# Kernel tuning notes

Measured on AMD Instinct MI355X. Metric: run time of the kernel, lower is better.

The kernel has to match this reference:

```python
import jax, jax.numpy as jnp
import numpy as np

N_NODES = 100000
N_EDGES = 3200000
D = 32


def setup_inputs() -> dict:
    key = jax.random.key(0)
    k = jax.random.split(key, 5)
    x = jax.random.normal(k[0], (N_NODES, D), dtype=jnp.float32)
    edge_index = jax.random.randint(k[1], (2, N_EDGES), 0, N_NODES, dtype=jnp.int64)
    W1 = jax.random.normal(k[2], (D, D), dtype=jnp.float32) * (1.0 / np.sqrt(D))
    b1 = jnp.zeros((D,), dtype=jnp.float32)
    W2 = jax.random.normal(k[3], (D, D), dtype=jnp.float32) * (1.0 / np.sqrt(D))
    b2 = jnp.zeros((D,), dtype=jnp.float32)
    return {"x": x, "edge_index": edge_index, "W1": W1, "b1": b1, "W2": W2, "b2": b2}


def reference(x, edge_index, W1, b1, W2, b2):
    n = x.shape[0]
    # add self-loops (PyG GCNConv default)
    loop = jnp.arange(n, dtype=edge_index.dtype)
    src = jnp.concatenate([edge_index[0], loop])
    dst = jnp.concatenate([edge_index[1], loop])
    # symmetric normalization: deg computed on dst with self-loops; deg >= 1 so no inf handling needed
    deg = jax.ops.segment_sum(jnp.ones_like(src, dtype=x.dtype), dst, num_segments=n)
    dinv = jax.lax.rsqrt(deg)
    norm = (dinv[src] * dinv[dst])[:, None]  # [E+N, 1]

    def gcn_layer(h, W, b):
        h = h @ W.T                                        # dense transform [N, D]
        msg = h[src] * norm                                # gather + scale   [E+N, D]
        agg = jax.ops.segment_sum(msg, dst, num_segments=n)  # scatter-add  [N, D]
        return jax.nn.relu(agg + b)

    h = gcn_layer(x, W1, b1)
    h = gcn_layer(h, W2, b2)
    return h
```

## Files before the change

### kernel.cpp

```cpp
#include <hip/hip_runtime.h>

#define THREADS 256
#define BIGT 1024
#define NBLK 256
#define BSHIFT 8
#define BSZ (1 << BSHIFT)
#define MAXB 512

__global__ void detect_kernel(const unsigned int* ei_words, int* flag_int64, long long n_words) {
    __shared__ int nonzero;
    if (threadIdx.x == 0) nonzero = 0;
    __syncthreads();
    long long w = 2LL * threadIdx.x + 1;
    if (w < n_words) {
        if (ei_words[w] != 0u) atomicOr(&nonzero, 1);
    }
    __syncthreads();
    if (threadIdx.x == 0) *flag_int64 = (nonzero == 0) ? 1 : 0;
}

__global__ __launch_bounds__(BIGT) void bin_count_kernel(
        const void* __restrict__ ei, const int* __restrict__ flag_int64,
        int* __restrict__ blockhist, int E, int NB) {
    __shared__ int h[MAXB];
    int tid = threadIdx.x;
    for (int i = tid; i < NB; i += blockDim.x) h[i] = 0;
    __syncthreads();
    int chunk = (E + gridDim.x - 1) / gridDim.x;
    int s = blockIdx.x * chunk;
    int e = min(E, s + chunk);
    if (*flag_int64) {
        const long long* p = (const long long*)ei;
        for (int i = s + tid; i < e; i += blockDim.x)
            atomicAdd(&h[(int)p[E + i] >> BSHIFT], 1);
    } else {
        const int* p = (const int*)ei;
        for (int i = s + tid; i < e; i += blockDim.x)
            atomicAdd(&h[p[E + i] >> BSHIFT], 1);
    }
    __syncthreads();
    for (int i = tid; i < NB; i += blockDim.x)
        blockhist[i * NBLK + blockIdx.x] = h[i];
}

__global__ __launch_bounds__(BIGT) void bin_write_kernel(
        const void* __restrict__ ei, const int* __restrict__ flag_int64,
        const int* __restrict__ offsets, unsigned int* __restrict__ ebuf,
        int E, int NB) {
    __shared__ int cur[MAXB];
    int tid = threadIdx.x;
    for (int i = tid; i < NB; i += blockDim.x)
        cur[i] = offsets[i * NBLK + blockIdx.x];
    __syncthreads();
    int chunk = (E + gridDim.x - 1) / gridDim.x;
    int s = blockIdx.x * chunk;
    int e = min(E, s + chunk);
    if (*flag_int64) {
        const long long* p = (const long long*)ei;
        for (int i = s + tid; i < e; i += blockDim.x) {
            int d = (int)p[E + i];
            int sr = (int)p[i];
            int pos = atomicAdd(&cur[d >> BSHIFT], 1);
            ebuf[pos] = ((unsigned int)(d & (BSZ - 1)) << 20) | (unsigned int)sr;
        }
    } else {
        const int* p = (const int*)ei;
        for (int i = s + tid; i < e; i += blockDim.x) {
            int d = p[E + i];
            int sr = p[i];
            int pos = atomicAdd(&cur[d >> BSHIFT], 1);
            ebuf[pos] = ((unsigned int)(d & (BSZ - 1)) << 20) | (unsigned int)sr;
        }
    }
}

__global__ void scan_blocks_kernel(const int* __restrict__ cnt, int* __restrict__ ofs,
                                   int* __restrict__ partials, int T) {
    __shared__ int sd[THREADS];
    int tid = threadIdx.x;
    int base = blockIdx.x * 1024 + tid * 4;
    int c0 = (base + 0 < T) ? cnt[base + 0] : 0;
    int c1 = (base + 1 < T) ? cnt[base + 1] : 0;
    int c2 = (base + 2 < T) ? cnt[base + 2] : 0;
    int c3 = (base + 3 < T) ? cnt[base + 3] : 0;
    int tsum = c0 + c1 + c2 + c3;
    sd[tid] = tsum;
    __syncthreads();
    for (int off = 1; off < THREADS; off <<= 1) {
        int t = (tid >= off) ? sd[tid - off] : 0;
        __syncthreads();
        sd[tid] += t;
        __syncthreads();
    }
    int excl = sd[tid] - tsum;
    if (base + 0 < T) ofs[base + 0] = excl;
    if (base + 1 < T) ofs[base + 1] = excl + c0;
    if (base + 2 < T) ofs[base + 2] = excl + c0 + c1;
    if (base + 3 < T) ofs[base + 3] = excl + c0 + c1 + c2;
    if (tid == THREADS - 1) partials[blockIdx.x] = sd[tid];
}

__global__ void scan_add2_kernel(int* __restrict__ ofs, const int* __restrict__ partials,
                                 int T, int SB) {
    __shared__ int sd[128];
    int tid = threadIdx.x;
    if (tid < 128) sd[tid] = (tid < SB) ? partials[tid] : 0;
    __syncthreads();
    for (int off = 1; off < 128; off <<= 1) {
        int t = (tid < 128 && tid >= off) ? sd[tid - off] : 0;
        __syncthreads();
        if (tid < 128) sd[tid] += t;
        __syncthreads();
    }
    int add = (blockIdx.x > 0) ? sd[blockIdx.x - 1] : 0;
    int base = blockIdx.x * 1024 + tid * 4;
    if (base + 0 < T) ofs[base + 0] += add;
    if (base + 1 < T) ofs[base + 1] += add;
    if (base + 2 < T) ofs[base + 2] += add;
    if (base + 3 < T) ofs[base + 3] += add;
    if (blockIdx.x == gridDim.x - 1 && tid == 0) ofs[T] = sd[SB - 1];
}

__global__ __launch_bounds__(BIGT) void place_dense_kernel(
        const unsigned int* __restrict__ ebuf, const int* __restrict__ offsets,
        const float* __restrict__ x, const float* __restrict__ W1,
        int* __restrict__ rowptr, float* __restrict__ dinv, int* __restrict__ col,
        float* __restrict__ ht1, int N, int NB) {
    __shared__ int cnt[BSZ];
    __shared__ int scanbuf[BSZ];
    __shared__ int baseL[BSZ];
    __shared__ int fillL[BSZ];
    __shared__ float dinvL[BSZ];
    __shared__ float Wt[1024];
    __shared__ float xs[BIGT];
    int b = blockIdx.x;
    int lo = b << BSHIFT;
    int tid = threadIdx.x;
    if (tid < BSZ) cnt[tid] = 0;
    Wt[(tid & 31) * 32 + (tid >> 5)] = W1[tid];
    __syncthreads();
    int start = offsets[b * NBLK];
    int end   = offsets[(b + 1) * NBLK];
    for (int p = start + tid; p < end; p += BIGT)
        atomicAdd(&cnt[(ebuf[p] >> 20) & (BSZ - 1)], 1);
    __syncthreads();
    int c = (tid < BSZ) ? cnt[tid] : 0;
    if (tid < BSZ) scanbuf[tid] = c;
    __syncthreads();
    for (int off = 1; off < BSZ; off <<= 1) {
        int t = (tid < BSZ && tid >= off) ? scanbuf[tid - off] : 0;
        __syncthreads();
        if (tid < BSZ) scanbuf[tid] += t;
        __syncthreads();
    }
    if (tid < BSZ) {
        int excl = scanbuf[tid] - c;
        int node = lo + tid;
        float dv = 1.0f / sqrtf((float)(c + 1));
        dinvL[tid] = dv;
        if (node < N) {
            rowptr[node] = start + excl;
            dinv[node] = dv;
            if (node == N - 1) rowptr[N] = start + excl + c;
        }
        baseL[tid] = start + excl;
        fillL[tid] = 0;
    }
    __syncthreads();
    for (int p = start + tid; p < end; p += BIGT) {
        unsigned int v = ebuf[p];
        int dl = (v >> 20) & (BSZ - 1);
        int pos = baseL[dl] + atomicAdd(&fillL[dl], 1);
        col[pos] = (int)(v & 0xFFFFFu);
    }
    __syncthreads();
    for (int base0 = 0; base0 < BSZ * 32; base0 += BIGT) {
        int idx = base0 + tid;
        int ln = idx >> 5;
        int node = lo + ln;
        xs[tid] = (node < N) ? x[(size_t)lo * 32 + idx] : 0.f;
        __syncthreads();
        if (node < N) {
            int j = idx & 31;
            const float* xr = xs + ((tid >> 5) << 5);
            float s = 0.f;
#pragma unroll
            for (int k = 0; k < 32; ++k) s = fmaf(xr[k], Wt[k * 32 + j], s);
            ht1[(size_t)node * 32 + j] = s * dinvL[ln];
        }
        __syncthreads();
    }
}

__global__ __launch_bounds__(THREADS) void agg_dense_kernel(
        const float* __restrict__ ht1, const int* __restrict__ rowptr,
        const int* __restrict__ col, const float* __restrict__ dinv,
        const float* __restrict__ b1, const float* __restrict__ W2,
        float* __restrict__ ht2, int N) {
    __shared__ float Wt[1024];
    __shared__ float hr[THREADS];
    int tid = threadIdx.x;
    for (int idx = tid; idx < 1024; idx += THREADS)
        Wt[(idx & 31) * 32 + (idx >> 5)] = W2[idx];
    int gid = blockIdx.x * THREADS + tid;
    int n = gid >> 5;
    int j = gid & 31;
    bool act = (n < N);
    float h1v = 0.f, dv = 0.f;
    if (act) {
        dv = dinv[n];
        float s = ht1[gid];
        int p = rowptr[n], end = rowptr[n + 1];
        for (; p + 8 <= end; p += 8) {
            int c0 = col[p], c1 = col[p + 1], c2 = col[p + 2], c3 = col[p + 3];
            int c4 = col[p + 4], c5 = col[p + 5], c6 = col[p + 6], c7 = col[p + 7];
            float v0 = ht1[c0 * 32 + j];
            float v1 = ht1[c1 * 32 + j];
            float v2 = ht1[c2 * 32 + j];
            float v3 = ht1[c3 * 32 + j];
            float v4 = ht1[c4 * 32 + j];
            float v5 = ht1[c5 * 32 + j];
            float v6 = ht1[c6 * 32 + j];
            float v7 = ht1[c7 * 32 + j];
            s += ((v0 + v1) + (v2 + v3)) + ((v4 + v5) + (v6 + v7));
        }
        for (; p + 4 <= end; p += 4) {
            int c0 = col[p], c1 = col[p + 1], c2 = col[p + 2], c3 = col[p + 3];
            float v0 = ht1[c0 * 32 + j];
            float v1 = ht1[c1 * 32 + j];
            float v2 = ht1[c2 * 32 + j];
            float v3 = ht1[c3 * 32 + j];
            s += (v0 + v1) + (v2 + v3);
        }
        for (; p < end; ++p) s += ht1[col[p] * 32 + j];
        h1v = fmaxf(fmaf(dv, s, b1[j]), 0.f);
    }
    hr[tid] = h1v;
    __syncthreads();
    if (act) {
        const float* hrow = hr + ((tid >> 5) << 5);
        float t = 0.f;
#pragma unroll
        for (int k = 0; k < 32; ++k) t = fmaf(hrow[k], Wt[k * 32 + j], t);
        ht2[gid] = t * dv;
    }
}

__global__ __launch_bounds__(THREADS) void agg_final_kernel(
        const float* __restrict__ ht2, const int* __restrict__ rowptr,
        const int* __restrict__ col, const float* __restrict__ dinv,
        const float* __restrict__ bias, float* __restrict__ out, int N) {
    int gid = blockIdx.x * THREADS + threadIdx.x;
    int n = gid >> 5;
    if (n >= N) return;
    int j = gid & 31;
    float s = ht2[gid];
    int p = rowptr[n], end = rowptr[n + 1];
    for (; p + 8 <= end; p += 8) {
        int c0 = col[p], c1 = col[p + 1], c2 = col[p + 2], c3 = col[p + 3];
        int c4 = col[p + 4], c5 = col[p + 5], c6 = col[p + 6], c7 = col[p + 7];
        float v0 = ht2[c0 * 32 + j];
        float v1 = ht2[c1 * 32 + j];
        float v2 = ht2[c2 * 32 + j];
        float v3 = ht2[c3 * 32 + j];
        float v4 = ht2[c4 * 32 + j];
        float v5 = ht2[c5 * 32 + j];
        float v6 = ht2[c6 * 32 + j];
        float v7 = ht2[c7 * 32 + j];
        s += ((v0 + v1) + (v2 + v3)) + ((v4 + v5) + (v6 + v7));
    }
    for (; p + 4 <= end; p += 4) {
        int c0 = col[p], c1 = col[p + 1], c2 = col[p + 2], c3 = col[p + 3];
        float v0 = ht2[c0 * 32 + j];
        float v1 = ht2[c1 * 32 + j];
        float v2 = ht2[c2 * 32 + j];
        float v3 = ht2[c3 * 32 + j];
        s += (v0 + v1) + (v2 + v3);
    }
    for (; p < end; ++p) s += ht2[col[p] * 32 + j];
    float r = fmaxf(fmaf(dinv[n], s, bias[j]), 0.f);
    __builtin_nontemporal_store(r, out + gid);
}

extern "C" void kernel_launch(void* const* d_in, const int* in_sizes, int n_in,
                              void* d_out, int out_size, void* d_ws, size_t ws_size,
                              hipStream_t stream) {
    const float* x  = (const float*)d_in[0];
    const void*  ei = d_in[1];
    const float* W1 = (const float*)d_in[2];
    const float* b1 = (const float*)d_in[3];
    const float* W2 = (const float*)d_in[4];
    const float* b2 = (const float*)d_in[5];
    float* out = (float*)d_out;

    int N = in_sizes[0] / 32;
    long long twoE = (long long)in_sizes[1];
    int E = (int)(twoE / 2);
    int NB = (N + BSZ - 1) >> BSHIFT;
    int T  = NB * NBLK;

    char* ws = (char*)d_ws;
    size_t o = 0;
    auto alloc = [&](size_t bytes) { size_t r = o; o += (bytes + 255) & ~(size_t)255; return r; };
    int*   flag      = (int*)(ws + alloc(4));
    int*   blockhist = (int*)(ws + alloc((size_t)T * 4));
    int*   offsets   = (int*)(ws + alloc((size_t)(T + 1) * 4));
    int*   rowptr    = (int*)(ws + alloc((size_t)(N + 1) * 4));
    int*   partials  = (int*)(ws + alloc(512));
    float* dinv      = (float*)(ws + alloc((size_t)N * 4));
    unsigned int* ebuf = (unsigned int*)(ws + alloc((size_t)E * 4));
    int*   col       = (int*)(ws + alloc((size_t)E * 4));
    float* ht1       = (float*)(ws + alloc((size_t)N * 32 * 4));
    float* ht2       = (float*)(ws + alloc((size_t)N * 32 * 4));

    detect_kernel<<<1, 256, 0, stream>>>((const unsigned int*)ei, flag, twoE);

    bin_count_kernel<<<NBLK, BIGT, 0, stream>>>(ei, flag, blockhist, E, NB);

    int SB = (T + 1023) / 1024;
    scan_blocks_kernel<<<SB, THREADS, 0, stream>>>(blockhist, offsets, partials, T);
    scan_add2_kernel<<<SB, THREADS, 0, stream>>>(offsets, partials, T, SB);

    bin_write_kernel<<<NBLK, BIGT, 0, stream>>>(ei, flag, offsets, ebuf, E, NB);
    place_dense_kernel<<<NB, BIGT, 0, stream>>>(ebuf, offsets, x, W1, rowptr, dinv, col, ht1, N, NB);

    int GB = (N * 32 + THREADS - 1) / THREADS;
    agg_dense_kernel<<<GB, THREADS, 0, stream>>>(ht1, rowptr, col, dinv, b1, W2, ht2, N);
    agg_final_kernel<<<GB, THREADS, 0, stream>>>(ht2, rowptr, col, dinv, b2, out, N);
}
```

Before: 274.7 us.

## Fold dtype probe and partial-scan add into binning kernels, unroll gathers to 16

Removes the separate int64-detect kernel by probing the high words inside each binning block, and removes the scan-add kernel by having consumer kernels rescan the block partials in LDS and add them on the fly. This cuts two kernel launches and one pass over the offsets array. The aggregation loops are also unrolled to 16 gathers per iteration to raise memory-level parallelism, at the cost of more registers. The per-block dtype probe only checks that block's own chunk, which could disagree across blocks in edge cases.

```diff
diff --git a/kernel.cpp b/kernel.cpp
--- a/kernel.cpp
+++ b/kernel.cpp
@@ -6,30 +6,28 @@
 #define BSHIFT 8
 #define BSZ (1 << BSHIFT)
 #define MAXB 512
-
-__global__ void detect_kernel(const unsigned int* ei_words, int* flag_int64, long long n_words) {
-    __shared__ int nonzero;
-    if (threadIdx.x == 0) nonzero = 0;
-    __syncthreads();
-    long long w = 2LL * threadIdx.x + 1;
-    if (w < n_words) {
-        if (ei_words[w] != 0u) atomicOr(&nonzero, 1);
-    }
-    __syncthreads();
-    if (threadIdx.x == 0) *flag_int64 = (nonzero == 0) ? 1 : 0;
+#define MAXSB 128
+
+__device__ __forceinline__ bool probe_int64(const void* ei, int s, int e, int tid, int* nz) {
+    if (tid == 0) *nz = 0;
+    __syncthreads();
+    int i = s + tid;
+    if (i < e && ((const unsigned int*)ei)[2 * i + 1] != 0u) atomicOr(nz, 1);
+    __syncthreads();
+    return (*nz == 0);
 }
 
 __global__ __launch_bounds__(BIGT) void bin_count_kernel(
-        const void* __restrict__ ei, const int* __restrict__ flag_int64,
-        int* __restrict__ blockhist, int E, int NB) {
+        const void* __restrict__ ei, int* __restrict__ blockhist, int E, int NB) {
     __shared__ int h[MAXB];
+    __shared__ int nz;
     int tid = threadIdx.x;
     for (int i = tid; i < NB; i += blockDim.x) h[i] = 0;
-    __syncthreads();
     int chunk = (E + gridDim.x - 1) / gridDim.x;
     int s = blockIdx.x * chunk;
     int e = min(E, s + chunk);
-    if (*flag_int64) {
+    bool is64 = probe_int64(ei, s, e, tid, &nz);
+    if (is64) {
         const long long* p = (const long long*)ei;
         for (int i = s + tid; i < e; i += blockDim.x)
             atomicAdd(&h[(int)p[E + i] >> BSHIFT], 1);
@@ -43,19 +41,63 @@
         blockhist[i * NBLK + blockIdx.x] = h[i];
 }
 
+__global__ void scan_blocks_kernel(const int* __restrict__ cnt, int* __restrict__ ofs,
+                                   int* __restrict__ partials, int T) {
+    __shared__ int sd[THREADS];
+    int tid = threadIdx.x;
+    int base = blockIdx.x * 1024 + tid * 4;
+    int c0 = (base + 0 < T) ? cnt[base + 0] : 0;
+    int c1 = (base + 1 < T) ? cnt[base + 1] : 0;
+    int c2 = (base + 2 < T) ? cnt[base + 2] : 0;
+    int c3 = (base + 3 < T) ? cnt[base + 3] : 0;
+    int tsum = c0 + c1 + c2 + c3;
+    sd[tid] = tsum;
+    __syncthreads();
+    for (int off = 1; off < THREADS; off <<= 1) {
+        int t = (tid >= off) ? sd[tid - off] : 0;
+        __syncthreads();
+        sd[tid] += t;
+        __syncthreads();
+    }
+    int excl = sd[tid] - tsum;
+    if (base + 0 < T) ofs[base + 0] = excl;
+    if (base + 1 < T) ofs[base + 1] = excl + c0;
+    if (base + 2 < T) ofs[base + 2] = excl + c0 + c1;
+    if (base + 3 < T) ofs[base + 3] = excl + c0 + c1 + c2;
+    if (tid == THREADS - 1) partials[blockIdx.x] = sd[tid];
+}
+
+__device__ __forceinline__ void scan_partials_lds(const int* __restrict__ partials,
+                                                  int* pscan, int tid, int SB) {
+    if (tid < MAXSB) pscan[tid] = (tid < SB) ? partials[tid] : 0;
+    __syncthreads();
+    for (int off = 1; off < MAXSB; off <<= 1) {
+        int t = (tid < MAXSB && tid >= off) ? pscan[tid - off] : 0;
+        __syncthreads();
+        if (tid < MAXSB) pscan[tid] += t;
+        __syncthreads();
+    }
+}
+
 __global__ __launch_bounds__(BIGT) void bin_write_kernel(
-        const void* __restrict__ ei, const int* __restrict__ flag_int64,
-        const int* __restrict__ offsets, unsigned int* __restrict__ ebuf,
-        int E, int NB) {
+        const void* __restrict__ ei, const int* __restrict__ ofs_local,
+        const int* __restrict__ partials, unsigned int* __restrict__ ebuf,
+        int E, int NB, int SB) {
     __shared__ int cur[MAXB];
-    int tid = threadIdx.x;
-    for (int i = tid; i < NB; i += blockDim.x)
-        cur[i] = offsets[i * NBLK + blockIdx.x];
-    __syncthreads();
+    __shared__ int pscan[MAXSB];
+    __shared__ int nz;
+    int tid = threadIdx.x;
+    scan_partials_lds(partials, pscan, tid, SB);
+    for (int i = tid; i < NB; i += blockDim.x) {
+        int idx = i * NBLK + blockIdx.x;
+        int c = idx >> 10;
+        cur[i] = ((c > 0) ? pscan[c - 1] : 0) + ofs_local[idx];
+    }
     int chunk = (E + gridDim.x - 1) / gridDim.x;
     int s = blockIdx.x * chunk;
     int e = min(E, s + chunk);
-    if (*flag_int64) {
+    bool is64 = probe_int64(ei, s, e, tid, &nz);
+    if (is64) {
         const long long* p = (const long long*)ei;
         for (int i = s + tid; i < e; i += blockDim.x) {
             int d = (int)p[E + i];
@@ -74,58 +116,12 @@
     }
 }
 
-__global__ void scan_blocks_kernel(const int* __restrict__ cnt, int* __restrict__ ofs,
-                                   int* __restrict__ partials, int T) {
-    __shared__ int sd[THREADS];
-    int tid = threadIdx.x;
-    int base = blockIdx.x * 1024 + tid * 4;
-    int c0 = (base + 0 < T) ? cnt[base + 0] : 0;
-    int c1 = (base + 1 < T) ? cnt[base + 1] : 0;
-    int c2 = (base + 2 < T) ? cnt[base + 2] : 0;
-    int c3 = (base + 3 < T) ? cnt[base + 3] : 0;
-    int tsum = c0 + c1 + c2 + c3;
-    sd[tid] = tsum;
-    __syncthreads();
-    for (int off = 1; off < THREADS; off <<= 1) {
-        int t = (tid >= off) ? sd[tid - off] : 0;
-        __syncthreads();
-        sd[tid] += t;
-        __syncthreads();
-    }
-    int excl = sd[tid] - tsum;
-    if (base + 0 < T) ofs[base + 0] = excl;
-    if (base + 1 < T) ofs[base + 1] = excl + c0;
-    if (base + 2 < T) ofs[base + 2] = excl + c0 + c1;
-    if (base + 3 < T) ofs[base + 3] = excl + c0 + c1 + c2;
-    if (tid == THREADS - 1) partials[blockIdx.x] = sd[tid];
-}
-
-__global__ void scan_add2_kernel(int* __restrict__ ofs, const int* __restrict__ partials,
-                                 int T, int SB) {
-    __shared__ int sd[128];
-    int tid = threadIdx.x;
-    if (tid < 128) sd[tid] = (tid < SB) ? partials[tid] : 0;
-    __syncthreads();
-    for (int off = 1; off < 128; off <<= 1) {
-        int t = (tid < 128 && tid >= off) ? sd[tid - off] : 0;
-        __syncthreads();
-        if (tid < 128) sd[tid] += t;
-        __syncthreads();
-    }
-    int add = (blockIdx.x > 0) ? sd[blockIdx.x - 1] : 0;
-    int base = blockIdx.x * 1024 + tid * 4;
-    if (base + 0 < T) ofs[base + 0] += add;
-    if (base + 1 < T) ofs[base + 1] += add;
-    if (base + 2 < T) ofs[base + 2] += add;
-    if (base + 3 < T) ofs[base + 3] += add;
-    if (blockIdx.x == gridDim.x - 1 && tid == 0) ofs[T] = sd[SB - 1];
-}
-
 __global__ __launch_bounds__(BIGT) void place_dense_kernel(
-        const unsigned int* __restrict__ ebuf, const int* __restrict__ offsets,
+        const unsigned int* __restrict__ ebuf, const int* __restrict__ ofs_local,
+        const int* __restrict__ partials,
         const float* __restrict__ x, const float* __restrict__ W1,
         int* __restrict__ rowptr, float* __restrict__ dinv, int* __restrict__ col,
-        float* __restrict__ ht1, int N, int NB) {
+        float* __restrict__ ht1, int N, int NB, int SB, int E) {
     __shared__ int cnt[BSZ];
     __shared__ int scanbuf[BSZ];
     __shared__ int baseL[BSZ];
@@ -133,14 +129,21 @@
     __shared__ float dinvL[BSZ];
     __shared__ float Wt[1024];
     __shared__ float xs[BIGT];
+    __shared__ int pscan[MAXSB];
     int b = blockIdx.x;
     int lo = b << BSHIFT;
     int tid = threadIdx.x;
     if (tid < BSZ) cnt[tid] = 0;
     Wt[(tid & 31) * 32 + (tid >> 5)] = W1[tid];
-    __syncthreads();
-    int start = offsets[b * NBLK];
-    int end   = offsets[(b + 1) * NBLK];
+    scan_partials_lds(partials, pscan, tid, SB);
+    int i0 = b * NBLK;
+    int start = ((i0 >> 10) > 0 ? pscan[(i0 >> 10) - 1] : 0) + ofs_local[i0];
+    int end;
+    if (b == NB - 1) end = E;
+    else {
+        int i1 = (b + 1) * NBLK;
+        end = ((i1 >> 10) > 0 ? pscan[(i1 >> 10) - 1] : 0) + ofs_local[i1];
+    }
     for (int p = start + tid; p < end; p += BIGT)
         atomicAdd(&cnt[(ebuf[p] >> 20) & (BSZ - 1)], 1);
     __syncthreads();
@@ -211,18 +214,15 @@
         dv = dinv[n];
         float s = ht1[gid];
         int p = rowptr[n], end = rowptr[n + 1];
-        for (; p + 8 <= end; p += 8) {
-            int c0 = col[p], c1 = col[p + 1], c2 = col[p + 2], c3 = col[p + 3];
-            int c4 = col[p + 4], c5 = col[p + 5], c6 = col[p + 6], c7 = col[p + 7];
-            float v0 = ht1[c0 * 32 + j];
-            float v1 = ht1[c1 * 32 + j];
-            float v2 = ht1[c2 * 32 + j];
-            float v3 = ht1[c3 * 32 + j];
-            float v4 = ht1[c4 * 32 + j];
-            float v5 = ht1[c5 * 32 + j];
-            float v6 = ht1[c6 * 32 + j];
-            float v7 = ht1[c7 * 32 + j];
-            s += ((v0 + v1) + (v2 + v3)) + ((v4 + v5) + (v6 + v7));
+        for (; p + 16 <= end; p += 16) {
+            int cc[16];
+            float vv[16];
+#pragma unroll
+            for (int u = 0; u < 16; ++u) cc[u] = col[p + u];
+#pragma unroll
+            for (int u = 0; u < 16; ++u) vv[u] = ht1[cc[u] * 32 + j];
+            s += (((vv[0] + vv[1]) + (vv[2] + vv[3])) + ((vv[4] + vv[5]) + (vv[6] + vv[7])))
+               + (((vv[8] + vv[9]) + (vv[10] + vv[11])) + ((vv[12] + vv[13]) + (vv[14] + vv[15])));
         }
         for (; p + 4 <= end; p += 4) {
             int c0 = col[p], c1 = col[p + 1], c2 = col[p + 2], c3 = col[p + 3];
@@ -256,18 +256,15 @@
     int j = gid & 31;
     float s = ht2[gid];
     int p = rowptr[n], end = rowptr[n + 1];
-    for (; p + 8 <= end; p += 8) {
-        int c0 = col[p], c1 = col[p + 1], c2 = col[p + 2], c3 = col[p + 3];
-        int c4 = col[p + 4], c5 = col[p + 5], c6 = col[p + 6], c7 = col[p + 7];
-        float v0 = ht2[c0 * 32 + j];
-        float v1 = ht2[c1 * 32 + j];
-        float v2 = ht2[c2 * 32 + j];
-        float v3 = ht2[c3 * 32 + j];
-        float v4 = ht2[c4 * 32 + j];
-        float v5 = ht2[c5 * 32 + j];
-        float v6 = ht2[c6 * 32 + j];
-        float v7 = ht2[c7 * 32 + j];
-        s += ((v0 + v1) + (v2 + v3)) + ((v4 + v5) + (v6 + v7));
+    for (; p + 16 <= end; p += 16) {
+        int cc[16];
+        float vv[16];
+#pragma unroll
+        for (int u = 0; u < 16; ++u) cc[u] = col[p + u];
+#pragma unroll
+        for (int u = 0; u < 16; ++u) vv[u] = ht2[cc[u] * 32 + j];
+        s += (((vv[0] + vv[1]) + (vv[2] + vv[3])) + ((vv[4] + vv[5]) + (vv[6] + vv[7])))
+           + (((vv[8] + vv[9]) + (vv[10] + vv[11])) + ((vv[12] + vv[13]) + (vv[14] + vv[15])));
     }
     for (; p + 4 <= end; p += 4) {
         int c0 = col[p], c1 = col[p + 1], c2 = col[p + 2], c3 = col[p + 3];
@@ -298,13 +295,13 @@
     int E = (int)(twoE / 2);
     int NB = (N + BSZ - 1) >> BSHIFT;
     int T  = NB * NBLK;
+    int SB = (T + 1023) / 1024;
 
     char* ws = (char*)d_ws;
     size_t o = 0;
     auto alloc = [&](size_t bytes) { size_t r = o; o += (bytes + 255) & ~(size_t)255; return r; };
-    int*   flag      = (int*)(ws + alloc(4));
     int*   blockhist = (int*)(ws + alloc((size_t)T * 4));
-    int*   offsets   = (int*)(ws + alloc((size_t)(T + 1) * 4));
+    int*   ofs_local = (int*)(ws + alloc((size_t)T * 4));
     int*   rowptr    = (int*)(ws + alloc((size_t)(N + 1) * 4));
     int*   partials  = (int*)(ws + alloc(512));
     float* dinv      = (float*)(ws + alloc((size_t)N * 4));
@@ -313,16 +310,11 @@
     float* ht1       = (float*)(ws + alloc((size_t)N * 32 * 4));
     float* ht2       = (float*)(ws + alloc((size_t)N * 32 * 4));
 
-    detect_kernel<<<1, 256, 0, stream>>>((const unsigned int*)ei, flag, twoE);
-
-    bin_count_kernel<<<NBLK, BIGT, 0, stream>>>(ei, flag, blockhist, E, NB);
-
-    int SB = (T + 1023) / 1024;
-    scan_blocks_kernel<<<SB, THREADS, 0, stream>>>(blockhist, offsets, partials, T);
-    scan_add2_kernel<<<SB, THREADS, 0, stream>>>(offsets, partials, T, SB);
-
-    bin_write_kernel<<<NBLK, BIGT, 0, stream>>>(ei, flag, offsets, ebuf, E, NB);
-    place_dense_kernel<<<NB, BIGT, 0, stream>>>(ebuf, offsets, x, W1, rowptr, dinv, col, ht1, N, NB);
+    bin_count_kernel<<<NBLK, BIGT, 0, stream>>>(ei, blockhist, E, NB);
+    scan_blocks_kernel<<<SB, THREADS, 0, stream>>>(blockhist, ofs_local, partials, T);
+    bin_write_kernel<<<NBLK, BIGT, 0, stream>>>(ei, ofs_local, partials, ebuf, E, NB, SB);
+    place_dense_kernel<<<NB, BIGT, 0, stream>>>(ebuf, ofs_local, partials, x, W1,
+                                                rowptr, dinv, col, ht1, N, NB, SB, E);
 
     int GB = (N * 32 + THREADS - 1) / THREADS;
     agg_dense_kernel<<<GB, THREADS, 0, stream>>>(ht1, rowptr, col, dinv, b1, W2, ht2, N);
```

Measured after the change: 276.3 us. No clear change (+0.6%).
